# Kernel optimization log

Measured on AMD Instinct MI355X. Metric: run time of the kernel, lower is better.

The kernel has to match this reference:

```python
import jax, jax.numpy as jnp
import numpy as np

B, T, C, H, L, V = 2, 1024, 768, 12, 12, 50257
D = C // H  # head size = 64
EPS = 1e-5


def _layer_norm(x, w, b):
    m = x.mean(-1, keepdims=True)
    v = x.var(-1, keepdims=True)
    return (x - m) * jax.lax.rsqrt(v + EPS) * w + b


def setup_inputs() -> dict:
    key = jax.random.key(0)
    ks = jax.random.split(key, 8)
    std = 0.02
    res_std = 0.02 * (2 * L) ** -0.5  # NANOGPT_SCALE_INIT
    rn = lambda k, shape, s: jax.random.normal(k, shape, jnp.float32) * s
    return dict(
        idx=jax.random.randint(ks[0], (B, T), 0, V),
        wte=rn(ks[1], (V, C), std),
        wpe=rn(ks[2], (T, C), std),
        ln1_w=jnp.ones((L, C), jnp.float32), ln1_b=jnp.zeros((L, C), jnp.float32),
        qkv_w=rn(ks[3], (L, C, 3 * C), std), qkv_b=jnp.zeros((L, 3 * C), jnp.float32),
        proj_w=rn(ks[4], (L, C, C), res_std), proj_b=jnp.zeros((L, C), jnp.float32),
        ln2_w=jnp.ones((L, C), jnp.float32), ln2_b=jnp.zeros((L, C), jnp.float32),
        fc_w=rn(ks[5], (L, C, 4 * C), std), fc_b=jnp.zeros((L, 4 * C), jnp.float32),
        fco_w=rn(ks[6], (L, 4 * C, C), res_std), fco_b=jnp.zeros((L, C), jnp.float32),
        lnf_w=jnp.ones((C,), jnp.float32), lnf_b=jnp.zeros((C,), jnp.float32),
    )


def reference(idx, wte, wpe, ln1_w, ln1_b, qkv_w, qkv_b, proj_w, proj_b,
              ln2_w, ln2_b, fc_w, fc_b, fco_w, fco_b, lnf_w, lnf_b):
    x = wte[idx] + wpe[:T]  # [B, T, C] tok + pos emb
    mask = jnp.tril(jnp.ones((T, T), bool))  # causal
    scale = 1.0 / np.sqrt(D).astype(np.float32)

    def block(x, p):
        l1w, l1b, qw, qb, pw, pb, l2w, l2b, fw, fb, fow, fob = p
        h = _layer_norm(x, l1w, l1b)
        qkv = h @ qw + qb  # [B, T, 3C]
        q, k, v = jnp.split(qkv, 3, axis=-1)
        q = q.reshape(B, T, H, D)
        k = k.reshape(B, T, H, D)
        v = v.reshape(B, T, H, D)
        att = jnp.einsum('bqhd,bkhd->bhqk', q, k) * scale
        att = jnp.where(mask, att, -jnp.inf)
        att = jax.nn.softmax(att, axis=-1)
        y = jnp.einsum('bhqk,bkhd->bqhd', att, v).reshape(B, T, C)
        x = x + y @ pw + pb
        h2 = _layer_norm(x, l2w, l2b)
        x = x + jax.nn.gelu(h2 @ fw + fb, approximate=True) @ fow + fob
        return x, None

    x, _ = jax.lax.scan(block, x, (ln1_w, ln1_b, qkv_w, qkv_b, proj_w, proj_b,
                                   ln2_w, ln2_b, fc_w, fc_b, fco_w, fco_b))
    x = _layer_norm(x, lnf_w, lnf_b)
    logits = x @ wte.T  # tied lm_head
    return logits
```

## Files before the change

kernel.cpp:

```cpp
#include <hip/hip_runtime.h>
#include <cmath>
#include <cstdint>

#define T_SEQ 1024
#define NH 12
#define NL 12
#define NV 50257
#define CD 768
#define M_ROWS 2048

typedef __bf16 bf16_t;
typedef __bf16 bf16x4 __attribute__((ext_vector_type(4)));
typedef __bf16 bf16x8 __attribute__((ext_vector_type(8)));
typedef float f32x4 __attribute__((ext_vector_type(4)));

__device__ __forceinline__ void gload16(const bf16_t* g, bf16_t* l) {
  __builtin_amdgcn_global_load_lds(
      (const __attribute__((address_space(1))) void*)g,
      (__attribute__((address_space(3))) void*)l, 16, 0, 0);
}

__global__ __launch_bounds__(256) void embed_k(const int* __restrict__ idx,
    const float* __restrict__ wte, const float* __restrict__ wpe,
    float* __restrict__ x) {
  int m = blockIdx.x;
  int t = m & (T_SEQ - 1);
  int tok = idx[m];
  const float* a = wte + (size_t)tok * CD;
  const float* p = wpe + (size_t)t * CD;
  float* xr = x + (size_t)m * CD;
  int c = threadIdx.x;
  xr[c]       = a[c]       + p[c];
  xr[c + 256] = a[c + 256] + p[c + 256];
  xr[c + 512] = a[c + 512] + p[c + 512];
}

__global__ __launch_bounds__(256) void cvt_k(const float* __restrict__ in,
    bf16_t* __restrict__ out, int n4) {
  int i = blockIdx.x * 256 + threadIdx.x;
  if (i < n4) {
    float4 v = ((const float4*)in)[i];
    bf16_t* o = out + (size_t)i * 4;
    o[0] = (bf16_t)v.x; o[1] = (bf16_t)v.y;
    o[2] = (bf16_t)v.z; o[3] = (bf16_t)v.w;
  }
}

__global__ __launch_bounds__(256) void transcvt_k(const float* __restrict__ W0,
    bf16_t* __restrict__ WT0, int K, int N) {
  const float* W = W0 + (size_t)blockIdx.z * K * N;
  bf16_t* WT = WT0 + (size_t)blockIdx.z * N * K;
  __shared__ float tl[32][33];
  int k0 = blockIdx.y * 32, n0 = blockIdx.x * 32;
  int j = threadIdx.x & 31, i0 = threadIdx.x >> 5;
  #pragma unroll
  for (int i = i0; i < 32; i += 8) tl[i][j] = W[(size_t)(k0 + i) * N + n0 + j];
  __syncthreads();
  #pragma unroll
  for (int i = i0; i < 32; i += 8)
    WT[(size_t)(n0 + i) * K + k0 + j] = (bf16_t)tl[j][i];
}

__global__ __launch_bounds__(256) void ln_k(const float* __restrict__ x,
    const float* __restrict__ w, const float* __restrict__ bi,
    bf16_t* __restrict__ out) {
  int row = blockIdx.x;
  const float* xr = x + (size_t)row * CD;
  int t = threadIdx.x;
  float v0 = xr[t], v1 = xr[t + 256], v2 = xr[t + 512];
  float s = v0 + v1 + v2;
  float ss = v0 * v0 + v1 * v1 + v2 * v2;
  #pragma unroll
  for (int o = 1; o < 64; o <<= 1) { s += __shfl_xor(s, o); ss += __shfl_xor(ss, o); }
  __shared__ float sh[8];
  int wid = t >> 6, lane = t & 63;
  if (lane == 0) { sh[wid] = s; sh[4 + wid] = ss; }
  __syncthreads();
  s  = sh[0] + sh[1] + sh[2] + sh[3];
  ss = sh[4] + sh[5] + sh[6] + sh[7];
  float mean = s * (1.f / CD);
  float var  = ss * (1.f / CD) - mean * mean;
  float rs = rsqrtf(var + 1e-5f);
  bf16_t* orow = out + (size_t)row * CD;
  orow[t]       = (bf16_t)((v0 - mean) * rs * w[t]       + bi[t]);
  orow[t + 256] = (bf16_t)((v1 - mean) * rs * w[t + 256] + bi[t + 256]);
  orow[t + 512] = (bf16_t)((v2 - mean) * rs * w[t + 512] + bi[t + 512]);
}

template <int BM, int BN, int BK, int EPI, bool FUSEVT>
__global__ __launch_bounds__(256) void gemm_bt(
    const bf16_t* __restrict__ A,
    const bf16_t* __restrict__ BT,
    const float* __restrict__ bias,
    const float* __restrict__ resid,
    void* __restrict__ out_p,
    bf16_t* __restrict__ vt,
    int Mdim, int Ndim, int Kdim) {
  constexpr int MR = BM / 32, NR = BN / 32;
  constexpr int KS = BK / 32;
  constexpr int LPW = (BM + BN) * BK / 2048;
  __shared__ __align__(1024) bf16_t As[3][BM * BK];
  __shared__ __align__(1024) bf16_t Bs[3][BN * BK];
  const int t = threadIdx.x;
  const int wid = t >> 6, lane = t & 63;
  const int wm = wid >> 1, wn = wid & 1;
  const int m0 = blockIdx.y * BM, n0 = blockIdx.x * BN;
  const int l15 = lane & 15, lhi = lane >> 4;

  auto stage = [&](int bi, int kt) {
    if (BK == 32) {
      const int srow = lane >> 2, schk = lane & 3;
      #pragma unroll
      for (int i = 0; i < BM / 64; ++i) {
        int rbase = wid * (BM / 4) + i * 16;
        int r = rbase + srow;
        int c = schk ^ ((r >> 1) & 3);
        gload16(A + (size_t)(m0 + r) * Kdim + kt + c * 8, &As[bi][rbase * 32]);
      }
      #pragma unroll
      for (int i = 0; i < BN / 64; ++i) {
        int rbase = wid * (BN / 4) + i * 16;
        int r = rbase + srow;
        int nr = n0 + r; if (nr >= Ndim) nr = Ndim - 1;
        int c = schk ^ ((r >> 1) & 3);
        gload16(BT + (size_t)nr * Kdim + kt + c * 8, &Bs[bi][rbase * 32]);
      }
    } else {
      const int srow = lane >> 3, schk = lane & 7;
      #pragma unroll
      for (int i = 0; i < BM / 32; ++i) {
        int rbase = wid * (BM / 4) + i * 8;
        int r = rbase + srow;
        int c = schk ^ (r & 7);
        gload16(A + (size_t)(m0 + r) * Kdim + kt + c * 8, &As[bi][rbase * 64]);
      }
      #pragma unroll
      for (int i = 0; i < BN / 32; ++i) {
        int rbase = wid * (BN / 4) + i * 8;
        int r = rbase + srow;
        int nr = n0 + r; if (nr >= Ndim) nr = Ndim - 1;
        int c = schk ^ (r & 7);
        gload16(BT + (size_t)nr * Kdim + kt + c * 8, &Bs[bi][rbase * 64]);
      }
    }
  };

  f32x4 acc[MR][NR] = {};
  const int NT = Kdim / BK;

  stage(0, 0);
  if (NT > 1) stage(1, BK);
  for (int tt = 0; tt < NT; ++tt) {
    if (tt < NT - 1) asm volatile("s_waitcnt vmcnt(%0)" :: "i"(LPW) : "memory");
    else             asm volatile("s_waitcnt vmcnt(0)" ::: "memory");
    __builtin_amdgcn_sched_barrier(0);
    __builtin_amdgcn_s_barrier();
    __builtin_amdgcn_sched_barrier(0);

    const bf16_t* Ab = As[tt % 3];
    const bf16_t* Bb = Bs[tt % 3];
    bf16x8 af[KS][MR], bfr[KS][NR];
    #pragma unroll
    for (int ks = 0; ks < KS; ++ks) {
      #pragma unroll
      for (int mm = 0; mm < MR; ++mm) {
        int ra = wm * (BM / 2) + mm * 16 + l15;
        int ch = (BK == 32) ? ((lhi ^ (ra >> 1)) & 3) : ((ks * 4 + lhi) ^ (ra & 7));
        af[ks][mm] = *(const bf16x8*)&Ab[ra * BK + ch * 8];
      }
      #pragma unroll
      for (int nn = 0; nn < NR; ++nn) {
        int rb = wn * (BN / 2) + nn * 16 + l15;
        int ch = (BK == 32) ? ((lhi ^ (rb >> 1)) & 3) : ((ks * 4 + lhi) ^ (rb & 7));
        bfr[ks][nn] = *(const bf16x8*)&Bb[rb * BK + ch * 8];
      }
    }
    if (tt + 2 < NT) stage((tt + 2) % 3, (tt + 2) * BK);

    __builtin_amdgcn_s_setprio(1);
    #pragma unroll
    for (int ks = 0; ks < KS; ++ks)
      #pragma unroll
      for (int mm = 0; mm < MR; ++mm)
        #pragma unroll
        for (int nn = 0; nn < NR; ++nn)
          acc[mm][nn] = __builtin_amdgcn_mfma_f32_16x16x32_bf16(
              af[ks][mm], bfr[ks][nn], acc[mm][nn], 0, 0, 0);
    __builtin_amdgcn_s_setprio(0);

    __builtin_amdgcn_sched_barrier(0);
    __builtin_amdgcn_s_barrier();
    __builtin_amdgcn_sched_barrier(0);
  }

  bf16_t* ob = (bf16_t*)out_p;
  float*  of = (float*)out_p;
  const int row0 = m0 + wm * (BM / 2);
  const int col0 = n0 + wn * (BN / 2);
  #pragma unroll
  for (int mm = 0; mm < MR; ++mm) {
    #pragma unroll
    for (int nn = 0; nn < NR; ++nn) {
      int col = col0 + nn * 16 + l15;
      if (col >= Ndim) continue;
      float bv = (EPI != 3) ? bias[col] : 0.f;
      if (EPI == 0) {
        bf16_t vv[4];
        #pragma unroll
        for (int r = 0; r < 4; ++r) {
          int row = row0 + mm * 16 + lhi * 4 + r;
          float v = acc[mm][nn][r] + bv;
          vv[r] = (bf16_t)v;
          ob[(size_t)row * Ndim + col] = vv[r];
        }
        if (FUSEVT && col >= 2 * CD) {
          int h = (col - 2 * CD) >> 6;
          int d = (col - 2 * CD) & 63;
          int brow = row0 + mm * 16 + lhi * 4;
          int bh = (brow >> 10) * NH + h;
          int tt0 = brow & (T_SEQ - 1);
          *(bf16x4*)&vt[((size_t)bh * 64 + d) * T_SEQ + tt0] = *(const bf16x4*)vv;
        }
      } else {
        #pragma unroll
        for (int r = 0; r < 4; ++r) {
          int row = row0 + mm * 16 + lhi * 4 + r;
          float v = acc[mm][nn][r] + bv;
          size_t o = (size_t)row * Ndim + col;
          if (EPI == 1) {
            float u = v + 0.044715f * v * v * v;
            v = 0.5f * v * (1.f + tanhf(0.79788456080286536f * u));
            ob[o] = (bf16_t)v;
          } else if (EPI == 2) {
            of[o] = resid[o] + v;
          } else {
            of[o] = v;
          }
        }
      }
    }
  }
}

#define LMH_GY 197
__global__ __launch_bounds__(512, 2) void gemm_lm(
    const bf16_t* __restrict__ A,
    const bf16_t* __restrict__ BT,
    float* __restrict__ out) {
  __shared__ __align__(1024) bf16_t As[4][256 * 32];
  __shared__ __align__(1024) bf16_t Bs[4][256 * 32];
  const int t = threadIdx.x;
  const int wid = t >> 6, lane = t & 63;
  const int wr = wid >> 2, wc = wid & 3;
  const int l15 = lane & 15, lhi = lane >> 4;
  const int srow = lane >> 2;
  const int schk = lane & 3;

  int lin = blockIdx.x;
  int swz = (lin & 7) * LMH_GY + (lin >> 3);
  const int m0 = (swz & 7) * 256;
  const int n0 = (swz >> 3) * 256;

  auto stage = [&](int bi, int kt) {
    #pragma unroll
    for (int hf = 0; hf < 2; ++hf) {
      int rb = hf * 128 + wid * 16;
      int r = rb + srow;
      int c = schk ^ ((r >> 1) & 3);
      gload16(A + (size_t)(m0 + r) * CD + kt * 32 + c * 8, &As[bi][rb * 32]);
    }
    #pragma unroll
    for (int hf = 0; hf < 2; ++hf) {
      int rb = hf * 128 + wid * 16;
      int r = rb + srow;
      int nr = n0 + r; if (nr >= NV) nr = NV - 1;
      int c = schk ^ ((r >> 1) & 3);
      gload16(BT + (size_t)nr * CD + kt * 32 + c * 8, &Bs[bi][rb * 32]);
    }
  };

  f32x4 acc[8][4] = {};
  const int NT = CD / 32;

  stage(0, 0); stage(1, 1); stage(2, 2);
  for (int tt = 0; tt < NT; ++tt) {
    if (tt < NT - 2)       asm volatile("s_waitcnt vmcnt(8)" ::: "memory");
    else if (tt == NT - 2) asm volatile("s_waitcnt vmcnt(4)" ::: "memory");
    else                   asm volatile("s_waitcnt vmcnt(0)" ::: "memory");
    __builtin_amdgcn_sched_barrier(0);
    __builtin_amdgcn_s_barrier();
    __builtin_amdgcn_sched_barrier(0);

    const bf16_t* Ab = As[tt & 3];
    const bf16_t* Bb = Bs[tt & 3];
    bf16x8 af[8], bfr[4];
    #pragma unroll
    for (int mm = 0; mm < 8; ++mm) {
      int ra = wr * 128 + mm * 16 + l15;
      af[mm] = *(const bf16x8*)&Ab[ra * 32 + ((lhi ^ (ra >> 1)) & 3) * 8];
    }
    #pragma unroll
    for (int nn = 0; nn < 4; ++nn) {
      int rb = wc * 64 + nn * 16 + l15;
      bfr[nn] = *(const bf16x8*)&Bb[rb * 32 + ((lhi ^ (rb >> 1)) & 3) * 8];
    }
    if (tt + 3 < NT) stage((tt + 3) & 3, tt + 3);

    __builtin_amdgcn_s_setprio(1);
    #pragma unroll
    for (int mm = 0; mm < 8; ++mm)
      #pragma unroll
      for (int nn = 0; nn < 4; ++nn)
        acc[mm][nn] = __builtin_amdgcn_mfma_f32_16x16x32_bf16(af[mm], bfr[nn], acc[mm][nn], 0, 0, 0);
    __builtin_amdgcn_s_setprio(0);

    __builtin_amdgcn_sched_barrier(0);
    __builtin_amdgcn_s_barrier();
    __builtin_amdgcn_sched_barrier(0);
  }

  const int row0 = m0 + wr * 128;
  const int col0 = n0 + wc * 64;
  #pragma unroll
  for (int mm = 0; mm < 8; ++mm) {
    #pragma unroll
    for (int nn = 0; nn < 4; ++nn) {
      int col = col0 + nn * 16 + l15;
      if (col >= NV) continue;
      #pragma unroll
      for (int r = 0; r < 4; ++r)
        out[(size_t)(row0 + mm * 16 + lhi * 4 + r) * NV + col] = acc[mm][nn][r];
    }
  }
}

__global__ __launch_bounds__(64) void attn_k(const bf16_t* __restrict__ qkv,
                                             const bf16_t* __restrict__ VT,
                                             bf16_t* __restrict__ y) {
  __shared__ __align__(16) bf16_t Ps[16 * 40];
  const int lane = threadIdx.x;
  const int gw = blockIdx.x;
  const int qi = gw & 63;
  const int bh = gw >> 6;
  const int h = bh % NH, b = bh / NH;
  const bf16_t* Qbase = qkv + (size_t)b * T_SEQ * (3 * CD) + h * 64;
  const bf16_t* Kbase = Qbase + CD;
  const bf16_t* Vt = VT + (size_t)bh * 64 * T_SEQ;

  const int l15 = lane & 15, lhi = lane >> 4;
  const int q0 = qi * 16;

  bf16x8 aq[2];
  #pragma unroll
  for (int c = 0; c < 2; ++c)
    aq[c] = *(const bf16x8*)(Qbase + (size_t)(q0 + l15) * (3 * CD) + c * 32 + lhi * 8);

  f32x4 acc[4] = {};
  float m_[4], l_[4];
  #pragma unroll
  for (int r = 0; r < 4; ++r) { m_[r] = -INFINITY; l_[r] = 0.f; }

  const int qrow = q0 + lhi * 4;
  const int nt = (q0 + 47) / 32;
  for (int kt = 0; kt < nt; ++kt) {
    const int k0 = kt * 32;
    f32x4 s[2] = {};
    #pragma unroll
    for (int c = 0; c < 2; ++c) {
      #pragma unroll
      for (int kc = 0; kc < 2; ++kc) {
        bf16x8 bk = *(const bf16x8*)(Kbase + (size_t)(k0 + kc * 16 + l15) * (3 * CD) + c * 32 + lhi * 8);
        s[kc] = __builtin_amdgcn_mfma_f32_16x16x32_bf16(aq[c], bk, s[kc], 0, 0, 0);
      }
    }
    float mx[4];
    #pragma unroll
    for (int r = 0; r < 4; ++r) mx[r] = -INFINITY;
    #pragma unroll
    for (int kc = 0; kc < 2; ++kc) {
      const int kcol = k0 + kc * 16 + l15;
      #pragma unroll
      for (int r = 0; r < 4; ++r) {
        float sv = (kcol <= qrow + r) ? s[kc][r] * 0.125f : -INFINITY;
        s[kc][r] = sv;
        mx[r] = fmaxf(mx[r], sv);
      }
    }
    #pragma unroll
    for (int r = 0; r < 4; ++r) {
      mx[r] = fmaxf(mx[r], __shfl_xor(mx[r], 1));
      mx[r] = fmaxf(mx[r], __shfl_xor(mx[r], 2));
      mx[r] = fmaxf(mx[r], __shfl_xor(mx[r], 4));
      mx[r] = fmaxf(mx[r], __shfl_xor(mx[r], 8));
    }
    float al[4], rs[4];
    #pragma unroll
    for (int r = 0; r < 4; ++r) {
      float mn = fmaxf(m_[r], mx[r]);
      al[r] = __expf(m_[r] - mn);
      m_[r] = mn;
      float p0 = __expf(s[0][r] - mn);
      float p1 = __expf(s[1][r] - mn);
      s[0][r] = p0; s[1][r] = p1;
      rs[r] = p0 + p1;
    }
    #pragma unroll
    for (int r = 0; r < 4; ++r) {
      rs[r] += __shfl_xor(rs[r], 1);
      rs[r] += __shfl_xor(rs[r], 2);
      rs[r] += __shfl_xor(rs[r], 4);
      rs[r] += __shfl_xor(rs[r], 8);
      l_[r] = l_[r] * al[r] + rs[r];
    }
    #pragma unroll
    for (int dt = 0; dt < 4; ++dt)
      #pragma unroll
      for (int r = 0; r < 4; ++r) acc[dt][r] *= al[r];
    #pragma unroll
    for (int kc = 0; kc < 2; ++kc)
      #pragma unroll
      for (int r = 0; r < 4; ++r)
        Ps[(lhi * 4 + r) * 40 + kc * 16 + l15] = (bf16_t)s[kc][r];
    bf16x8 pa = *(const bf16x8*)&Ps[l15 * 40 + lhi * 8];
    #pragma unroll
    for (int dt = 0; dt < 4; ++dt) {
      bf16x8 bv = *(const bf16x8*)(Vt + (size_t)(dt * 16 + l15) * T_SEQ + k0 + lhi * 8);
      acc[dt] = __builtin_amdgcn_mfma_f32_16x16x32_bf16(pa, bv, acc[dt], 0, 0, 0);
    }
  }
  #pragma unroll
  for (int dt = 0; dt < 4; ++dt)
    #pragma unroll
    for (int r = 0; r < 4; ++r)
      y[(size_t)(b * T_SEQ + q0 + lhi * 4 + r) * CD + h * 64 + dt * 16 + l15] =
          (bf16_t)(acc[dt][r] / l_[r]);
}

extern "C" void kernel_launch(void* const* d_in, const int* in_sizes, int n_in,
                              void* d_out, int out_size, void* d_ws, size_t ws_size,
                              hipStream_t stream) {
  const int*   idx   = (const int*)d_in[0];
  const float* wte   = (const float*)d_in[1];
  const float* wpe   = (const float*)d_in[2];
  const float* ln1w  = (const float*)d_in[3];
  const float* ln1b  = (const float*)d_in[4];
  const float* qkvw  = (const float*)d_in[5];
  const float* qkvb  = (const float*)d_in[6];
  const float* projw = (const float*)d_in[7];
  const float* projb = (const float*)d_in[8];
  const float* ln2w  = (const float*)d_in[9];
  const float* ln2b  = (const float*)d_in[10];
  const float* fcw   = (const float*)d_in[11];
  const float* fcb   = (const float*)d_in[12];
  const float* fcow  = (const float*)d_in[13];
  const float* fcob  = (const float*)d_in[14];
  const float* lnfw  = (const float*)d_in[15];
  const float* lnfb  = (const float*)d_in[16];
  float* out = (float*)d_out;

  char* w = (char*)d_ws;
  auto alloc = [&](size_t bytes) {
    char* p = w; w += (bytes + 255) & ~(size_t)255; return p;
  };
  float*  x     = (float*)alloc((size_t)M_ROWS * CD * 4);
  float*  x2    = (float*)alloc((size_t)M_ROWS * CD * 4);
  bf16_t* hb    = (bf16_t*)alloc((size_t)M_ROWS * CD * 2);
  bf16_t* qkvB  = (bf16_t*)alloc((size_t)M_ROWS * 3 * CD * 2);
  bf16_t* yb    = (bf16_t*)alloc((size_t)M_ROWS * CD * 2);
  bf16_t* fca   = (bf16_t*)alloc((size_t)M_ROWS * 4 * CD * 2);
  bf16_t* VT    = (bf16_t*)alloc((size_t)2 * NH * 64 * T_SEQ * 2);
  bf16_t* wteB  = (bf16_t*)alloc((size_t)NV * CD * 2);
  bf16_t* wqT_s = (bf16_t*)alloc((size_t)3 * CD * CD * 2);
  bf16_t* wpT_s = (bf16_t*)alloc((size_t)CD * CD * 2);
  bf16_t* wfT_s = (bf16_t*)alloc((size_t)4 * CD * CD * 2);
  bf16_t* woT_s = (bf16_t*)alloc((size_t)CD * 4 * CD * 2);
  const size_t qkvSz = (size_t)3 * CD * CD, prSz = (size_t)CD * CD;
  const size_t fcSz  = (size_t)4 * CD * CD, foSz = (size_t)CD * 4 * CD;
  bf16_t* wqT_b = (bf16_t*)alloc(NL * qkvSz * 2);
  bf16_t* wpT_b = (bf16_t*)alloc(NL * prSz * 2);
  bf16_t* wfT_b = (bf16_t*)alloc(NL * fcSz * 2);
  bf16_t* woT_b = (bf16_t*)alloc(NL * foSz * 2);
  const bool big = (size_t)(w - (char*)d_ws) <= ws_size;

  embed_k<<<M_ROWS, 256, 0, stream>>>(idx, wte, wpe, x);
  {
    int n4 = NV * CD / 4;
    cvt_k<<<(n4 + 255) / 256, 256, 0, stream>>>(wte, wteB, n4);
  }
  if (big) {
    transcvt_k<<<dim3(3 * CD / 32, CD / 32, NL), 256, 0, stream>>>(qkvw,  wqT_b, CD, 3 * CD);
    transcvt_k<<<dim3(CD / 32, CD / 32, NL),     256, 0, stream>>>(projw, wpT_b, CD, CD);
    transcvt_k<<<dim3(4 * CD / 32, CD / 32, NL), 256, 0, stream>>>(fcw,   wfT_b, CD, 4 * CD);
    transcvt_k<<<dim3(CD / 32, 4 * CD / 32, NL), 256, 0, stream>>>(fcow,  woT_b, 4 * CD, CD);
  }

  for (int l = 0; l < NL; ++l) {
    bf16_t *wqT, *wpT, *wfT, *woT;
    if (big) {
      wqT = wqT_b + (size_t)l * qkvSz; wpT = wpT_b + (size_t)l * prSz;
      wfT = wfT_b + (size_t)l * fcSz;  woT = woT_b + (size_t)l * foSz;
    } else {
      wqT = wqT_s; wpT = wpT_s; wfT = wfT_s; woT = woT_s;
      transcvt_k<<<dim3(3 * CD / 32, CD / 32, 1), 256, 0, stream>>>(qkvw  + (size_t)l * CD * 3 * CD, wqT, CD, 3 * CD);
      transcvt_k<<<dim3(CD / 32, CD / 32, 1),     256, 0, stream>>>(projw + (size_t)l * CD * CD,     wpT, CD, CD);
      transcvt_k<<<dim3(4 * CD / 32, CD / 32, 1), 256, 0, stream>>>(fcw   + (size_t)l * CD * 4 * CD, wfT, CD, 4 * CD);
      transcvt_k<<<dim3(CD / 32, 4 * CD / 32, 1), 256, 0, stream>>>(fcow  + (size_t)l * 4 * CD * CD, woT, 4 * CD, CD);
    }

    ln_k<<<M_ROWS, 256, 0, stream>>>(x, ln1w + l * CD, ln1b + l * CD, hb);
    gemm_bt<128, 128, 32, 0, true><<<dim3(3 * CD / 128, M_ROWS / 128), 256, 0, stream>>>(
        hb, wqT, qkvb + l * 3 * CD, nullptr, qkvB, VT, M_ROWS, 3 * CD, CD);
    attn_k<<<2 * NH * 64, 64, 0, stream>>>(qkvB, VT, yb);
    gemm_bt<64, 64, 32, 2, false><<<dim3(CD / 64, M_ROWS / 64), 256, 0, stream>>>(
        yb, wpT, projb + l * CD, x, x2, nullptr, M_ROWS, CD, CD);
    ln_k<<<M_ROWS, 256, 0, stream>>>(x2, ln2w + l * CD, ln2b + l * CD, hb);
    gemm_bt<128, 128, 32, 1, false><<<dim3(4 * CD / 128, M_ROWS / 128), 256, 0, stream>>>(
        hb, wfT, fcb + l * 4 * CD, nullptr, fca, nullptr, M_ROWS, 4 * CD, CD);
    gemm_bt<64, 64, 64, 2, false><<<dim3(CD / 64, M_ROWS / 64), 256, 0, stream>>>(
        fca, woT, fcob + l * CD, x2, x, nullptr, M_ROWS, CD, 4 * CD);
  }

  ln_k<<<M_ROWS, 256, 0, stream>>>(x, lnfw, lnfb, hb);
  gemm_lm<<<8 * LMH_GY, 512, 0, stream>>>(hb, wteB, out);
}
```

Before: 2.178 ms.

## Retile LM-head GEMM to 256x64, use sigmoid GELU, widen proj K-tile

The LM-head GEMM moves from 512-thread 256x256 tiles with a 4-stage pipeline to 256-thread 256x64 tiles with a 3-stage pipeline. That quadruples the block count, improving load balance across CUs and cutting LDS use per block, but it re-reads the A operand (and its global loads) for every 64-column tile. The GELU epilogue replaces tanhf with the identity 0.5(1+tanh(z)) = sigmoid(2z), computed with __expf, which is a cheaper transcendental. The attention projection GEMM's K tile goes from 32 to 64.

```diff
diff --git a/kernel.cpp b/kernel.cpp
--- a/kernel.cpp
+++ b/kernel.cpp
@@ -229,7 +229,8 @@
           size_t o = (size_t)row * Ndim + col;
           if (EPI == 1) {
             float u = v + 0.044715f * v * v * v;
-            v = 0.5f * v * (1.f + tanhf(0.79788456080286536f * u));
+            float w2 = 1.59576912f * u;
+            v = v / (1.f + __expf(-w2));
             ob[o] = (bf16_t)v;
           } else if (EPI == 2) {
             of[o] = resid[o] + v;
@@ -242,16 +243,15 @@
   }
 }
 
-#define LMH_GY 197
-__global__ __launch_bounds__(512, 2) void gemm_lm(
+#define LMH_GY 786
+__global__ __launch_bounds__(256) void gemm_lm(
     const bf16_t* __restrict__ A,
     const bf16_t* __restrict__ BT,
     float* __restrict__ out) {
-  __shared__ __align__(1024) bf16_t As[4][256 * 32];
-  __shared__ __align__(1024) bf16_t Bs[4][256 * 32];
+  __shared__ __align__(1024) bf16_t As[3][256 * 32];
+  __shared__ __align__(1024) bf16_t Bs[3][64 * 32];
   const int t = threadIdx.x;
   const int wid = t >> 6, lane = t & 63;
-  const int wr = wid >> 2, wc = wid & 3;
   const int l15 = lane & 15, lhi = lane >> 4;
   const int srow = lane >> 2;
   const int schk = lane & 3;
@@ -259,56 +259,54 @@
   int lin = blockIdx.x;
   int swz = (lin & 7) * LMH_GY + (lin >> 3);
   const int m0 = (swz & 7) * 256;
-  const int n0 = (swz >> 3) * 256;
+  const int n0 = (swz >> 3) * 64;
 
   auto stage = [&](int bi, int kt) {
     #pragma unroll
-    for (int hf = 0; hf < 2; ++hf) {
-      int rb = hf * 128 + wid * 16;
-      int r = rb + srow;
+    for (int i = 0; i < 4; ++i) {
+      int rbase = wid * 64 + i * 16;
+      int r = rbase + srow;
       int c = schk ^ ((r >> 1) & 3);
-      gload16(A + (size_t)(m0 + r) * CD + kt * 32 + c * 8, &As[bi][rb * 32]);
-    }
-    #pragma unroll
-    for (int hf = 0; hf < 2; ++hf) {
-      int rb = hf * 128 + wid * 16;
-      int r = rb + srow;
+      gload16(A + (size_t)(m0 + r) * CD + kt * 32 + c * 8, &As[bi][rbase * 32]);
+    }
+    {
+      int rbase = wid * 16;
+      int r = rbase + srow;
       int nr = n0 + r; if (nr >= NV) nr = NV - 1;
       int c = schk ^ ((r >> 1) & 3);
-      gload16(BT + (size_t)nr * CD + kt * 32 + c * 8, &Bs[bi][rb * 32]);
+      gload16(BT + (size_t)nr * CD + kt * 32 + c * 8, &Bs[bi][rbase * 32]);
     }
   };
 
-  f32x4 acc[8][4] = {};
+  f32x4 acc[4][4] = {};
   const int NT = CD / 32;
 
-  stage(0, 0); stage(1, 1); stage(2, 2);
+  stage(0, 0); stage(1, 1);
   for (int tt = 0; tt < NT; ++tt) {
-    if (tt < NT - 2)       asm volatile("s_waitcnt vmcnt(8)" ::: "memory");
-    else if (tt == NT - 2) asm volatile("s_waitcnt vmcnt(4)" ::: "memory");
-    else                   asm volatile("s_waitcnt vmcnt(0)" ::: "memory");
+    if (tt < NT - 1) asm volatile("s_waitcnt vmcnt(5)" ::: "memory");
+    else             asm volatile("s_waitcnt vmcnt(0)" ::: "memory");
     __builtin_amdgcn_sched_barrier(0);
     __builtin_amdgcn_s_barrier();
     __builtin_amdgcn_sched_barrier(0);
 
-    const bf16_t* Ab = As[tt & 3];
-    const bf16_t* Bb = Bs[tt & 3];
-    bf16x8 af[8], bfr[4];
-    #pragma unroll
-    for (int mm = 0; mm < 8; ++mm) {
-      int ra = wr * 128 + mm * 16 + l15;
+    const bf16_t* Ab = As[tt % 3];
+    const bf16_t* Bb = Bs[tt % 3];
+    bf16x8 af[4], bfr[4];
+    #pragma unroll
+    for (int mm = 0; mm < 4; ++mm) {
+      int ra = wid * 64 + mm * 16 + l15;
       af[mm] = *(const bf16x8*)&Ab[ra * 32 + ((lhi ^ (ra >> 1)) & 3) * 8];
     }
     #pragma unroll
     for (int nn = 0; nn < 4; ++nn) {
-      int rb = wc * 64 + nn * 16 + l15;
+      int rb = nn * 16 + l15;
       bfr[nn] = *(const bf16x8*)&Bb[rb * 32 + ((lhi ^ (rb >> 1)) & 3) * 8];
     }
-    if (tt + 3 < NT) stage((tt + 3) & 3, tt + 3);
+    if (tt + 2 < NT) stage((tt + 2) % 3, tt + 2);
 
     __builtin_amdgcn_s_setprio(1);
     #pragma unroll
-    for (int mm = 0; mm < 8; ++mm)
+    for (int mm = 0; mm < 4; ++mm)
       #pragma unroll
       for (int nn = 0; nn < 4; ++nn)
         acc[mm][nn] = __builtin_amdgcn_mfma_f32_16x16x32_bf16(af[mm], bfr[nn], acc[mm][nn], 0, 0, 0);
@@ -319,13 +317,12 @@
     __builtin_amdgcn_sched_barrier(0);
   }
 
-  const int row0 = m0 + wr * 128;
-  const int col0 = n0 + wc * 64;
-  #pragma unroll
-  for (int mm = 0; mm < 8; ++mm) {
+  const int row0 = m0 + wid * 64;
+  #pragma unroll
+  for (int mm = 0; mm < 4; ++mm) {
     #pragma unroll
     for (int nn = 0; nn < 4; ++nn) {
-      int col = col0 + nn * 16 + l15;
+      int col = n0 + nn * 16 + l15;
       if (col >= NV) continue;
       #pragma unroll
       for (int r = 0; r < 4; ++r)
@@ -511,7 +508,7 @@
     gemm_bt<128, 128, 32, 0, true><<<dim3(3 * CD / 128, M_ROWS / 128), 256, 0, stream>>>(
         hb, wqT, qkvb + l * 3 * CD, nullptr, qkvB, VT, M_ROWS, 3 * CD, CD);
     attn_k<<<2 * NH * 64, 64, 0, stream>>>(qkvB, VT, yb);
-    gemm_bt<64, 64, 32, 2, false><<<dim3(CD / 64, M_ROWS / 64), 256, 0, stream>>>(
+    gemm_bt<64, 64, 64, 2, false><<<dim3(CD / 64, M_ROWS / 64), 256, 0, stream>>>(
         yb, wpT, projb + l * CD, x, x2, nullptr, M_ROWS, CD, CD);
     ln_k<<<M_ROWS, 256, 0, stream>>>(x2, ln2w + l * CD, ln2b + l * CD, hb);
     gemm_bt<128, 128, 32, 1, false><<<dim3(4 * CD / 128, M_ROWS / 128), 256, 0, stream>>>(
@@ -521,5 +518,5 @@
   }
 
   ln_k<<<M_ROWS, 256, 0, stream>>>(x, lnfw, lnfb, hb);
-  gemm_lm<<<8 * LMH_GY, 512, 0, stream>>>(hb, wteB, out);
-}
+  gemm_lm<<<8 * LMH_GY, 256, 0, stream>>>(hb, wteB, out);
+}
```

Result: no change. 2.160 ms (-0.8%).
